# Optimization experiments

Measured on AMD Instinct MI355X. Metric: run time of the kernel, lower is better.

## Reference

```python
import jax, jax.numpy as jnp
import numpy as np
from jax import lax

POOL_K, POOL_S, FINAL, KNN = 5, 3, 6, 819  # pool size/stride, adaptive out, k_neighbors


def setup_inputs() -> dict:
    key = jax.random.key(0)
    k1, k2, k3 = jax.random.split(key, 3)
    return {
        "x": jax.random.normal(k1, (64, 3, 32, 32), jnp.float32),
        "conv_weight": jax.random.normal(k2, (2048, 3, 6, 6), jnp.float32) * 0.05,
        "conv_bias": jax.random.normal(k3, (1, 2048, 1, 1), jnp.float32),
    }


def lowestk_heaviside(x, k):
    # indicator of the k channel-wise smallest values: x < (k+1)-th smallest
    kth = jnp.sort(x, axis=1)[:, k:k + 1]  # [B,1,H,W]
    return (x < kth).astype(x.dtype)


def avg_pool_ceil(x, k, s):
    # torch avg_pool2d(ceil_mode=True, padding=0): partial windows clipped to
    # the input and divided by the number of valid elements.
    H, W = x.shape[2], x.shape[3]
    oh = -(-(H - k) // s) + 1
    ow = -(-(W - k) // s) + 1
    ph = max(0, (oh - 1) * s + k - H)
    pw = max(0, (ow - 1) * s + k - W)
    dims, strides = (1, 1, k, k), (1, 1, s, s)
    pad = ((0, 0), (0, 0), (0, ph), (0, pw))
    sums = lax.reduce_window(x, 0.0, lax.add, dims, strides, pad)
    cnt = lax.reduce_window(jnp.ones((1, 1, H, W), x.dtype), 0.0, lax.add,
                            dims, strides, pad)
    return sums / cnt


def adaptive_avg_pool2d(x, n):
    # torch adaptive bins: [floor(i*S/n), ceil((i+1)*S/n)); separable in H/W
    def pool_axis(y, axis):
        size = y.shape[axis]
        parts = []
        for i in range(n):
            s = (i * size) // n
            e = -(-((i + 1) * size) // n)
            parts.append(lax.slice_in_dim(y, s, e, axis=axis)
                         .mean(axis=axis, keepdims=True))
        return jnp.concatenate(parts, axis=axis)
    return pool_axis(pool_axis(x, 2), 3)


def reference(x, conv_weight, conv_bias):
    out = lax.conv_general_dilated(x, conv_weight, (1, 1), 'VALID',
                                   dimension_numbers=('NCHW', 'OIHW', 'NCHW'))

    def branch(z):
        m = lowestk_heaviside(z, KNN)            # [B,2048,27,27]
        m = avg_pool_ceil(m, POOL_K, POOL_S)     # [B,2048,9,9]
        return adaptive_avg_pool2d(m, FINAL)     # [B,2048,6,6]

    out1 = branch(-out + conv_bias)
    out2 = branch(out + conv_bias)
    return (out1, out2)
```

## Files before the change

### kernel.cpp

```cpp
#include <hip/hip_runtime.h>
#include <cstdint>
#include <cstddef>

#define RANK_K 819

typedef __attribute__((ext_vector_type(2)))  float f32x2;
typedef __attribute__((ext_vector_type(16))) float f32x16;

__device__ __forceinline__ f32x2 pk_fma_blo(f32x2 a, f32x2 bs, f32x2 c) {
  f32x2 d;
  asm("v_pk_fma_f32 %0, %1, %2, %3 op_sel_hi:[1,0,1]"
      : "=v"(d) : "v"(a), "s"(bs), "v"(c));
  return d;
}
__device__ __forceinline__ f32x2 pk_fma_bhi(f32x2 a, f32x2 bs, f32x2 c) {
  f32x2 d;
  asm("v_pk_fma_f32 %0, %1, %2, %3 op_sel:[0,1,0] op_sel_hi:[1,1,1]"
      : "=v"(d) : "v"(a), "s"(bs), "v"(c));
  return d;
}

__device__ __forceinline__ int zbin256(float z) {
  float t = (z + 8.0f) * 16.0f;
  t = t < 0.0f ? 0.0f : (t > 255.0f ? 255.0f : t);
  return (int)t;
}

__global__ __launch_bounds__(256) void net99_wtrans(const float* __restrict__ w,
                                                    f32x2* __restrict__ wt4) {
  int idx = blockIdx.x * 256 + threadIdx.x;
  if (idx < 108 * 1024) {
    int k = idx / 1024, cc = idx % 1024;
    int ic = k % 3, sp = k / 3, ky = sp / 6, kx = sp % 6;
    int wo = ic * 36 + ky * 6 + kx;
    f32x2 t;
    t.x = w[cc * 108 + wo];
    t.y = w[(cc + 1024) * 108 + wo];
    wt4[idx] = t;
  }
}

__global__ __launch_bounds__(256, 4) void net99_conv(const float* __restrict__ x,
                                                     const f32x2* __restrict__ wt4,
                                                     float* __restrict__ conv, int b0) {
  const int y  = blockIdx.x;
  const int ct = blockIdx.y;
  const int bl = blockIdx.z;
  const int b  = b0 + bl;
  const int tid = threadIdx.x;
  const int cpair = ct * 256 + tid;
  const f32x2* wtc = wt4 + cpair;
  f32x2 acc[27];
#pragma unroll
  for (int q = 0; q < 27; ++q) acc[q] = (f32x2)(0.0f);
#pragma unroll 1
  for (int ky = 0; ky < 6; ++ky) {
    const float* r0 = x + ((b * 3 + 0) * 32 + (y + ky)) * 32;
    const float* r1 = x + ((b * 3 + 1) * 32 + (y + ky)) * 32;
    const float* r2 = x + ((b * 3 + 2) * 32 + (y + ky)) * 32;
    f32x2 wv[6][3];
#pragma unroll
    for (int kx = 0; kx < 6; ++kx)
#pragma unroll
      for (int ic = 0; ic < 3; ++ic)
        wv[kx][ic] = wtc[(size_t)((ky * 6 + kx) * 3 + ic) * 1024];
    {
      f32x16 a0, a1, a2;
      asm volatile(
          "s_load_dwordx16 %0, %3, 0x0\n\t"
          "s_load_dwordx16 %1, %4, 0x0\n\t"
          "s_load_dwordx16 %2, %5, 0x0\n\t"
          "s_waitcnt lgkmcnt(0)"
          : "=&s"(a0), "=&s"(a1), "=&s"(a2)
          : "s"(r0), "s"(r1), "s"(r2));
      __builtin_amdgcn_sched_barrier(0);
#pragma unroll
      for (int m = 0; m < 16; ++m) {
        f32x2 p[3];
        p[0].x = a0[(m >> 1) * 2]; p[0].y = a0[(m >> 1) * 2 + 1];
        p[1].x = a1[(m >> 1) * 2]; p[1].y = a1[(m >> 1) * 2 + 1];
        p[2].x = a2[(m >> 1) * 2]; p[2].y = a2[(m >> 1) * 2 + 1];
#pragma unroll
        for (int ic = 0; ic < 3; ++ic) {
#pragma unroll
          for (int kx = 0; kx < 6; ++kx) {
            if (kx <= m) {
              const int q = m - kx;
              acc[q] = (m & 1) ? pk_fma_bhi(wv[kx][ic], p[ic], acc[q])
                               : pk_fma_blo(wv[kx][ic], p[ic], acc[q]);
            }
          }
        }
      }
    }
    {
      f32x16 c0, c1, c2;
      asm volatile(
          "s_load_dwordx16 %0, %3, 0x40\n\t"
          "s_load_dwordx16 %1, %4, 0x40\n\t"
          "s_load_dwordx16 %2, %5, 0x40\n\t"
          "s_waitcnt lgkmcnt(0)"
          : "=&s"(c0), "=&s"(c1), "=&s"(c2)
          : "s"(r0), "s"(r1), "s"(r2));
      __builtin_amdgcn_sched_barrier(0);
#pragma unroll
      for (int m = 16; m < 32; ++m) {
        const int mm = m - 16;
        f32x2 p[3];
        p[0].x = c0[(mm >> 1) * 2]; p[0].y = c0[(mm >> 1) * 2 + 1];
        p[1].x = c1[(mm >> 1) * 2]; p[1].y = c1[(mm >> 1) * 2 + 1];
        p[2].x = c2[(mm >> 1) * 2]; p[2].y = c2[(mm >> 1) * 2 + 1];
#pragma unroll
        for (int ic = 0; ic < 3; ++ic) {
#pragma unroll
          for (int kx = 0; kx < 6; ++kx) {
            const int q = m - kx;
            if (q <= 26) {
              acc[q] = (m & 1) ? pk_fma_bhi(wv[kx][ic], p[ic], acc[q])
                               : pk_fma_blo(wv[kx][ic], p[ic], acc[q]);
            }
          }
        }
      }
    }
  }
  float* dstbase = conv + ((size_t)(bl * 27 + y) * 27) * 2048;
#pragma unroll
  for (int q = 0; q < 27; ++q) {
    dstbase[(size_t)q * 2048 + cpair]        = acc[q].x;
    dstbase[(size_t)q * 2048 + cpair + 1024] = acc[q].y;
  }
}

__global__ __launch_bounds__(256) void net99_select(const float* __restrict__ conv,
                                                    const float* __restrict__ bias,
                                                    uint8_t* __restrict__ mskb, int b0) {
  const int bl = blockIdx.x / 365;
  const int g  = blockIdx.x % 365;
  const int p0 = 2 * g;
  const bool has1 = (p0 + 1) < 729;
  const int gb = b0 + bl;
  const int tid  = threadIdx.x;
  const int lane = tid & 63;
  const int wid  = tid >> 6;
  const int nst  = has1 ? 4 : 2;
  __shared__ uint32_t hist[4][256];
  __shared__ float    cand[4][512];
  __shared__ int      cnt[4];
  __shared__ int      sbin[4], sbelow[4];
  __shared__ float    skth[4];

  const float4* __restrict__ s0 =
      (const float4*)(conv + ((size_t)bl * 729 + p0) * 2048) + tid * 2;
  const float4* __restrict__ b4 = (const float4*)bias + tid * 2;
  float4 va0 = s0[0], vb0 = s0[1];
  float4 va1 = {}, vb1 = {};
  if (has1) { va1 = s0[512]; vb1 = s0[513]; }
  float4 ba = b4[0], bb = b4[1];

  (&hist[0][0])[tid]       = 0u;
  (&hist[0][0])[tid + 256] = 0u;
  (&hist[0][0])[tid + 512] = 0u;
  (&hist[0][0])[tid + 768] = 0u;
  if (tid < 4) cnt[tid] = 0;

  float z[4][8];
  {
    float bv[8] = {ba.x, ba.y, ba.z, ba.w, bb.x, bb.y, bb.z, bb.w};
    float v0[8] = {va0.x, va0.y, va0.z, va0.w, vb0.x, vb0.y, vb0.z, vb0.w};
    float v1[8] = {va1.x, va1.y, va1.z, va1.w, vb1.x, vb1.y, vb1.z, vb1.w};
#pragma unroll
    for (int j = 0; j < 8; ++j) {
      z[0][j] = bv[j] - v0[j];
      z[1][j] = bv[j] + v0[j];
      z[2][j] = bv[j] - v1[j];
      z[3][j] = bv[j] + v1[j];
    }
  }
  __syncthreads();
#pragma unroll
  for (int j = 0; j < 8; ++j) {
    atomicAdd(&hist[0][zbin256(z[0][j])], 1u);
    atomicAdd(&hist[1][zbin256(z[1][j])], 1u);
  }
  if (has1) {
#pragma unroll
    for (int j = 0; j < 8; ++j) {
      atomicAdd(&hist[2][zbin256(z[2][j])], 1u);
      atomicAdd(&hist[3][zbin256(z[3][j])], 1u);
    }
  }
  __syncthreads();
  if (wid < nst) {
    const int s = wid;
    int h[4];
#pragma unroll
    for (int t = 0; t < 4; ++t) h[t] = (int)hist[s][lane * 4 + t];
    int loc = h[0] + h[1] + h[2] + h[3];
    int inc = loc;
#pragma unroll
    for (int off = 1; off < 64; off <<= 1) {
      int u = __shfl_up(inc, off);
      if (lane >= off) inc += u;
    }
    int pre = inc - loc;
    if (pre <= RANK_K && RANK_K < pre + loc) {
      int cum = pre;
#pragma unroll
      for (int t = 0; t < 4; ++t) {
        if (RANK_K < cum + h[t]) { sbin[s] = lane * 4 + t; sbelow[s] = cum; break; }
        cum += h[t];
      }
    }
  }
  __syncthreads();
#pragma unroll
  for (int s = 0; s < 4; ++s) {
    if (s >= 2 && !has1) break;
    const int tb = sbin[s];
#pragma unroll
    for (int j = 0; j < 8; ++j) {
      if (zbin256(z[s][j]) == tb) {
        int u = atomicAdd(&cnt[s], 1);
        if (u < 512) cand[s][u] = z[s][j];
      }
    }
  }
  __syncthreads();
  if (wid < nst) {
    const int s = wid;
    int cN = cnt[s] < 512 ? cnt[s] : 512;
    int rloc = RANK_K - sbelow[s];
    for (int ci = lane; ci < cN; ci += 64) {
      float v = cand[s][ci]; int rk = 0;
      for (int j = 0; j < cN; ++j) {
        float u = cand[s][j];
        rk += (u < v) || (u == v && j < ci);
      }
      if (rk == rloc) skth[s] = v;
    }
  }
  __syncthreads();
  const size_t pix0 = (size_t)gb * 729 + p0;
  {
    uint32_t m0 = 0u, m1 = 0u;
    const float k0 = skth[0], k1 = skth[1];
#pragma unroll
    for (int j = 0; j < 8; ++j) {
      m0 |= (uint32_t)(z[0][j] < k0) << j;
      m1 |= (uint32_t)(z[1][j] < k1) << j;
    }
    mskb[pix0 * 256 + tid]                      = (uint8_t)m0;
    mskb[((size_t)64 * 729 + pix0) * 256 + tid] = (uint8_t)m1;
  }
  if (has1) {
    uint32_t m2 = 0u, m3 = 0u;
    const float k2 = skth[2], k3 = skth[3];
#pragma unroll
    for (int j = 0; j < 8; ++j) {
      m2 |= (uint32_t)(z[2][j] < k2) << j;
      m3 |= (uint32_t)(z[3][j] < k3) << j;
    }
    mskb[(pix0 + 1) * 256 + tid]                      = (uint8_t)m2;
    mskb[((size_t)64 * 729 + pix0 + 1) * 256 + tid]   = (uint8_t)m3;
  }
}

__global__ __launch_bounds__(256) void net99_pool(const uint32_t* __restrict__ msk,
                                                  float* __restrict__ out) {
  __shared__ uint32_t stage[729 * 8];
  const int blk = blockIdx.x;
  const int cg  = blk & 7;
  const int sb  = blk >> 3;
  const int tid = threadIdx.x;
  const uint32_t* src = msk + (size_t)sb * 729 * 64 + cg * 8;
  for (int i = tid; i < 729 * 8; i += 256) {
    int p = i >> 3, w = i & 7;
    stage[i] = src[(size_t)p * 64 + w];
  }
  __syncthreads();
  const int lw = tid >> 5, sel = tid & 31;
  uint32_t rbm[27];
  for (int y = 0; y < 27; ++y) {
    uint32_t rb = 0;
#pragma unroll
    for (int xx = 0; xx < 27; ++xx)
      rb |= ((stage[(y * 27 + xx) * 8 + lw] >> sel) & 1u) << xx;
    rbm[y] = rb;
  }
  constexpr uint32_t WM[9] = {0x1Fu, 0xF8u, 0x7C0u, 0x3E00u, 0x1F000u,
                              0xF8000u, 0x7C0000u, 0x3E00000u, 0x7000000u};
  constexpr int CC[9]  = {5, 5, 5, 5, 5, 5, 5, 5, 3};
  constexpr int BW0[6] = {0, 1, 3, 4, 6, 7};
  constexpr int BW1[6] = {1, 2, 4, 5, 7, 8};
  const int s = sb >> 6, b = sb & 63, c = cg * 256 + tid;
  float* dst = out + (size_t)s * 4718592 + (size_t)(b * 2048 + c) * 36;
  for (int i = 0; i < 6; ++i) {
    float P[2][9];
#pragma unroll
    for (int t = 0; t < 2; ++t) {
      int r  = t ? BW1[i] : BW0[i];
      int y0 = 3 * r;
      int y1 = (y0 + 5 > 27) ? 27 : y0 + 5;
      int cr = y1 - y0;
      int pp[9];
#pragma unroll
      for (int cx = 0; cx < 9; ++cx) pp[cx] = 0;
      for (int yy = y0; yy < y1; ++yy) {
        uint32_t rb = rbm[yy];
#pragma unroll
        for (int cx = 0; cx < 9; ++cx) pp[cx] += __popc(rb & WM[cx]);
      }
#pragma unroll
      for (int cx = 0; cx < 9; ++cx)
        P[t][cx] = (float)pp[cx] / (float)(cr * CC[cx]);
    }
    float M[9];
#pragma unroll
    for (int cx = 0; cx < 9; ++cx) M[cx] = (P[0][cx] + P[1][cx]) * 0.5f;
#pragma unroll
    for (int j = 0; j < 6; ++j)
      dst[i * 6 + j] = (M[BW0[j]] + M[BW1[j]]) * 0.5f;
  }
}

extern "C" void kernel_launch(void* const* d_in, const int* in_sizes, int n_in,
                              void* d_out, int out_size, void* d_ws, size_t ws_size,
                              hipStream_t stream) {
  const float* x    = (const float*)d_in[0];
  const float* w    = (const float*)d_in[1];
  const float* bias = (const float*)d_in[2];
  float* out = (float*)d_out;
  uint8_t* ws = (uint8_t*)d_ws;

  const size_t WT_BYTES   = (size_t)108 * 1024 * 8;
  const size_t MASK_OFF   = WT_BYTES;
  const size_t MASK_BYTES = (size_t)2 * 64 * 729 * 64 * 4;
  const size_t CONV_OFF   = MASK_OFF + MASK_BYTES;
  const size_t PER_B      = (size_t)2048 * 729 * 4;

  f32x2*    wt4  = (f32x2*)ws;
  uint8_t*  mskb = (uint8_t*)(ws + MASK_OFF);
  uint32_t* msk  = (uint32_t*)(ws + MASK_OFF);
  float*    conv = (float*)(ws + CONV_OFF);

  size_t avail = ws_size > CONV_OFF ? ws_size - CONV_OFF : 0;
  int Bc = (int)(avail / PER_B);
  if (Bc < 1) Bc = 1;
  if (Bc > 64) Bc = 64;

  hipLaunchKernelGGL(net99_wtrans, dim3((108 * 1024 + 255) / 256), dim3(256), 0, stream, w, wt4);
  for (int b0 = 0; b0 < 64; b0 += Bc) {
    int nb = (64 - b0 < Bc) ? (64 - b0) : Bc;
    hipLaunchKernelGGL(net99_conv, dim3(27, 4, nb), dim3(256), 0, stream, x, wt4, conv, b0);
    hipLaunchKernelGGL(net99_select, dim3(nb * 365), dim3(256), 0, stream, conv, bias, mskb, b0);
  }
  hipLaunchKernelGGL(net99_pool, dim3(1024), dim3(256), 0, stream, msk, out);
}
```

Baseline: 427.4 us.

## Software-pipeline conv and select across batch chunks in a fused kernel

Merges the conv and select kernels into one launch whose blocks are split by index: the first blocks run select on the previous batch chunk and the rest run conv on the next chunk. Two double-buffered conv slots of 20 images each let the memory-bound select overlap with the compute-bound conv. In exchange, the fused kernel inherits the combined register and LDS footprint and the launch bounds of both bodies. The chunk size is fixed at 20 and no longer derived from the workspace size, so it assumes a large enough workspace.

```diff
diff --git a/kernel.cpp b/kernel.cpp
--- a/kernel.cpp
+++ b/kernel.cpp
@@ -40,12 +40,13 @@
   }
 }
 
-__global__ __launch_bounds__(256, 4) void net99_conv(const float* __restrict__ x,
-                                                     const f32x2* __restrict__ wt4,
-                                                     float* __restrict__ conv, int b0) {
-  const int y  = blockIdx.x;
-  const int ct = blockIdx.y;
-  const int bl = blockIdx.z;
+__device__ __forceinline__ void conv_body(const float* __restrict__ x,
+                                          const f32x2* __restrict__ wt4,
+                                          float* __restrict__ conv,
+                                          int b0, int idx) {
+  const int y  = idx % 27;
+  const int ct = (idx / 27) & 3;
+  const int bl = idx / 108;
   const int b  = b0 + bl;
   const int tid = threadIdx.x;
   const int cpair = ct * 256 + tid;
@@ -132,11 +133,12 @@
   }
 }
 
-__global__ __launch_bounds__(256) void net99_select(const float* __restrict__ conv,
-                                                    const float* __restrict__ bias,
-                                                    uint8_t* __restrict__ mskb, int b0) {
-  const int bl = blockIdx.x / 365;
-  const int g  = blockIdx.x % 365;
+__device__ __forceinline__ void select_body(const float* __restrict__ conv,
+                                            const float* __restrict__ bias,
+                                            uint8_t* __restrict__ mskb,
+                                            int b0, int bid) {
+  const int bl = bid / 365;
+  const int g  = bid % 365;
   const int p0 = 2 * g;
   const bool has1 = (p0 + 1) < 729;
   const int gb = b0 + bl;
@@ -266,6 +268,21 @@
   }
 }
 
+__global__ __launch_bounds__(256, 4) void net99_fused(
+    const float* __restrict__ x, const f32x2* __restrict__ wt4,
+    const float* __restrict__ bias,
+    float* __restrict__ convW, const float* __restrict__ convR,
+    uint8_t* __restrict__ mskb,
+    int b0c, int b0s, int nbs) {
+  const int bid = blockIdx.x;
+  const int selBlocks = nbs * 365;
+  if (bid < selBlocks) {
+    select_body(convR, bias, mskb, b0s, bid);
+  } else {
+    conv_body(x, wt4, convW, b0c, bid - selBlocks);
+  }
+}
+
 __global__ __launch_bounds__(256) void net99_pool(const uint32_t* __restrict__ msk,
                                                   float* __restrict__ out) {
   __shared__ uint32_t stage[729 * 8];
@@ -338,22 +355,34 @@
   const size_t MASK_BYTES = (size_t)2 * 64 * 729 * 64 * 4;
   const size_t CONV_OFF   = MASK_OFF + MASK_BYTES;
   const size_t PER_B      = (size_t)2048 * 729 * 4;
+  const int    CH         = 20;
+  const size_t SLOT_BYTES = (size_t)CH * PER_B;
 
   f32x2*    wt4  = (f32x2*)ws;
   uint8_t*  mskb = (uint8_t*)(ws + MASK_OFF);
   uint32_t* msk  = (uint32_t*)(ws + MASK_OFF);
-  float*    conv = (float*)(ws + CONV_OFF);
-
-  size_t avail = ws_size > CONV_OFF ? ws_size - CONV_OFF : 0;
-  int Bc = (int)(avail / PER_B);
-  if (Bc < 1) Bc = 1;
-  if (Bc > 64) Bc = 64;
+  float*    slot0 = (float*)(ws + CONV_OFF);
+  float*    slot1 = (float*)(ws + CONV_OFF + SLOT_BYTES);
 
   hipLaunchKernelGGL(net99_wtrans, dim3((108 * 1024 + 255) / 256), dim3(256), 0, stream, w, wt4);
-  for (int b0 = 0; b0 < 64; b0 += Bc) {
-    int nb = (64 - b0 < Bc) ? (64 - b0) : Bc;
-    hipLaunchKernelGGL(net99_conv, dim3(27, 4, nb), dim3(256), 0, stream, x, wt4, conv, b0);
-    hipLaunchKernelGGL(net99_select, dim3(nb * 365), dim3(256), 0, stream, conv, bias, mskb, b0);
-  }
+
+  const int cstart[4] = {0, 20, 40, 60};
+  const int clen[4]   = {20, 20, 20, 4};
+  float* slotp[2] = {slot0, slot1};
+  hipLaunchKernelGGL(net99_fused, dim3(108 * clen[0]), dim3(256), 0, stream,
+                     x, wt4, bias, slotp[0], (const float*)slot0, mskb,
+                     cstart[0], 0, 0);
+  for (int i = 1; i < 4; ++i) {
+    float*       W = slotp[i & 1];
+    const float* R = slotp[(i - 1) & 1];
+    hipLaunchKernelGGL(net99_fused, dim3(365 * clen[i - 1] + 108 * clen[i]),
+                       dim3(256), 0, stream,
+                       x, wt4, bias, W, R, mskb,
+                       cstart[i], cstart[i - 1], clen[i - 1]);
+  }
+  hipLaunchKernelGGL(net99_fused, dim3(365 * clen[3]), dim3(256), 0, stream,
+                     x, wt4, bias, slotp[0], (const float*)slotp[1], mskb,
+                     0, cstart[3], clen[3]);
+
   hipLaunchKernelGGL(net99_pool, dim3(1024), dim3(256), 0, stream, msk, out);
 }
```

Result: slower. 493.7 us (+15.5%).
